# Kernel tuning notes

Measured on AMD Instinct MI355X. Metric: run time of the kernel, lower is better.

The kernel has to match this reference:

```python
import jax, jax.numpy as jnp
import numpy as np

B, T, F, U = 32, 2048, 1024, 512


def setup_inputs() -> dict:
    key = jax.random.key(0)
    k1, k2, k3, k4, k5 = jax.random.split(key, 5)
    return {
        "x": jax.random.normal(k1, (B, T, F), dtype=jnp.float32),
        "W": jax.random.normal(k2, (F, U), dtype=jnp.float32) / np.sqrt(F),
        "b": jnp.zeros((U,), dtype=jnp.float32),
        "transitions": jax.random.normal(k3, (U, U), dtype=jnp.float32),
        "left_boundary": jax.random.normal(k4, (U,), dtype=jnp.float32) * 0.1,
        "right_boundary": jax.random.normal(k5, (U,), dtype=jnp.float32) * 0.1,
    }


def _add_boundary_energy(potentials, start, end):
    # mask=None path: add start to first timestep, end to last timestep
    first = potentials[:, :1, :] + start[None, None, :]
    last = potentials[:, -1:, :] + end[None, None, :]
    return jnp.concatenate([first, potentials[:, 1:-1, :], last], axis=1)


def _crf_decode(potentials, transitions):
    # Viterbi decode (tfa.text.crf_decode), full sequence lengths.
    # potentials: [B, T, U], transitions: [U, U]
    state0 = potentials[:, 0]                       # [B, U]
    rest = jnp.swapaxes(potentials[:, 1:], 0, 1)    # [T-1, B, U]

    def fwd(state, pot_t):
        # scores[b, i, j] = state[b, i] + transitions[i, j]
        scores = state[:, :, None] + transitions[None, :, :]  # [B, U, U]
        bp = jnp.argmax(scores, axis=1).astype(jnp.int32)     # [B, U]
        new_state = jnp.max(scores, axis=1) + pot_t
        return new_state, bp

    final_state, bps = jax.lax.scan(fwd, state0, rest)  # bps: [T-1, B, U]
    last_tag = jnp.argmax(final_state, axis=-1).astype(jnp.int32)  # [B]

    def back(tag, bp):
        prev = jnp.take_along_axis(bp, tag[:, None], axis=1)[:, 0]
        return prev, prev

    _, tags = jax.lax.scan(back, last_tag, bps, reverse=True)  # [T-1, B]
    seq = jnp.concatenate([tags, last_tag[None, :]], axis=0)   # [T, B]
    return jnp.swapaxes(seq, 0, 1)                             # [B, T]


def reference(x, W, b, transitions, left_boundary, right_boundary):
    potentials = jnp.einsum("btf,fu->btu", x, W) + b           # Dense(units)
    potentials = _add_boundary_energy(potentials, left_boundary, right_boundary)
    sequence_lengths = jnp.full((x.shape[0],), x.shape[1], dtype=jnp.int64)
    viterbi_sequence = _crf_decode(potentials, transitions)
    return viterbi_sequence, potentials, sequence_lengths, transitions
```

## Files before the change

### kernel.cpp

```cpp
#include <hip/hip_runtime.h>
#include <cstddef>

#define U_DIM 512
#define T_DIM 2048
#define B_DIM 32
#define F_DIM 1024
#define M_DIM (B_DIM * T_DIM)
#define NBLK 8
#define UB (U_DIM / NBLK)

#define BM 128
#define BN 64
#define BK 16

__global__ __launch_bounds__(256) void gemm_kernel(
    const float* __restrict__ x, const float* __restrict__ W,
    const float* __restrict__ bias, const float* __restrict__ lb,
    const float* __restrict__ rb, float* __restrict__ out)
{
  __shared__ float As[BK][BM + 4];
  __shared__ float Bs[BK][BN];
  const int m0 = blockIdx.x * BM;
  const int n0 = blockIdx.y * BN;
  const int tid = threadIdx.x;
  const int tx = tid & 15;
  const int ty = tid >> 4;

  float acc[8][4];
#pragma unroll
  for (int i = 0; i < 8; ++i)
#pragma unroll
    for (int j = 0; j < 4; ++j) acc[i][j] = 0.f;

  for (int k0 = 0; k0 < F_DIM; k0 += BK) {
#pragma unroll
    for (int i = 0; i < 2; ++i) {
      int id = i * 256 + tid;
      int row = id >> 2;
      int c4 = (id & 3) << 2;
      float4 a = *(const float4*)(x + (size_t)(m0 + row) * F_DIM + k0 + c4);
      As[c4 + 0][row] = a.x;
      As[c4 + 1][row] = a.y;
      As[c4 + 2][row] = a.z;
      As[c4 + 3][row] = a.w;
    }
    {
      int krow = tid >> 4;
      int c4 = (tid & 15) << 2;
      *(float4*)(&Bs[krow][c4]) =
          *(const float4*)(W + (size_t)(k0 + krow) * U_DIM + n0 + c4);
    }
    __syncthreads();
#pragma unroll
    for (int k = 0; k < BK; ++k) {
      float a[8], bb[4];
#pragma unroll
      for (int i = 0; i < 8; ++i) a[i] = As[k][ty * 8 + i];
#pragma unroll
      for (int j = 0; j < 4; ++j) bb[j] = Bs[k][tx * 4 + j];
#pragma unroll
      for (int i = 0; i < 8; ++i)
#pragma unroll
        for (int j = 0; j < 4; ++j) acc[i][j] += a[i] * bb[j];
    }
    __syncthreads();
  }

#pragma unroll
  for (int i = 0; i < 8; ++i) {
    int m = m0 + ty * 8 + i;
    int t = m & (T_DIM - 1);
    float4 o;
#pragma unroll
    for (int j = 0; j < 4; ++j) {
      int n = n0 + tx * 4 + j;
      float v = acc[i][j] + bias[n];
      if (t == 0) v += lb[n];
      if (t == T_DIM - 1) v += rb[n];
      ((float*)&o)[j] = v;
    }
    *(float4*)(out + (size_t)m * U_DIM + n0 + tx * 4) = o;
  }
}

__global__ void aux_kernel(const float* __restrict__ tr, float* __restrict__ out_tr,
                           float* __restrict__ trT, float* __restrict__ seqlen)
{
  int idx = blockIdx.x * blockDim.x + threadIdx.x;
  if (idx < U_DIM * U_DIM) {
    float v = tr[idx];
    out_tr[idx] = v;
    int r = idx >> 9;
    int c = idx & 511;
    trT[(size_t)c * U_DIM + r] = v;
  }
  if (idx < B_DIM) seqlen[idx] = (float)T_DIM;
}

__global__ void init_kernel(unsigned int* __restrict__ flags)
{
  int i = blockIdx.x * blockDim.x + threadIdx.x;
  if (i < B_DIM * NBLK) flags[i] = 0u;
}

__global__ __launch_bounds__(512) void scan_kernel(
    const float* __restrict__ pot, const float* __restrict__ trT,
    float* __restrict__ stateBuf,
    unsigned int* __restrict__ flags,
    unsigned short* __restrict__ bp,
    float* __restrict__ outv)
{
  const int blk = blockIdx.x;
  const int b = blk & (B_DIM - 1);
  const int j = blk >> 5;
  const int tid = threadIdx.x;
  const int u_local = tid >> 3;
  const int vseg = tid & 7;
  const int u = j * UB + u_local;

  __shared__ float sh_state[U_DIM];
  __shared__ float sh_v[U_DIM];
  __shared__ int sh_i[U_DIM];

  float4 trreg[16];
  const float* trRow = trT + (size_t)u * U_DIM;
#pragma unroll
  for (int m = 0; m < 16; ++m)
    trreg[m] = *(const float4*)(trRow + vseg * 4 + m * 32);

  const float* potb = pot + (size_t)b * T_DIM * U_DIM;
  unsigned int* myflags = flags + b * NBLK;

  for (int t = 1; t < T_DIM; ++t) {
    float p_u = potb[(size_t)t * U_DIM + u];

    if (t > 1) {
      if (tid < NBLK) {
        while (__hip_atomic_load(&myflags[tid], __ATOMIC_RELAXED,
                                 __HIP_MEMORY_SCOPE_AGENT) < (unsigned)(t - 1)) {}
      }
      __syncthreads();
      sh_state[tid] = __hip_atomic_load(
          &stateBuf[(size_t)((t - 1) & 1) * B_DIM * U_DIM +
                    (size_t)b * U_DIM + tid],
          __ATOMIC_RELAXED, __HIP_MEMORY_SCOPE_AGENT);
    } else {
      sh_state[tid] = potb[tid];
    }
    __syncthreads();

    float best = -3.402823466e38f;
    int bi = 0;
#pragma unroll
    for (int m = 0; m < 16; ++m) {
      float4 st = *(const float4*)(&sh_state[vseg * 4 + m * 32]);
      float4 trv = trreg[m];
      int vbase = vseg * 4 + m * 32;
      float s0 = st.x + trv.x;
      float s1 = st.y + trv.y;
      float s2 = st.z + trv.z;
      float s3 = st.w + trv.w;
      if (s0 > best) { best = s0; bi = vbase; }
      if (s1 > best) { best = s1; bi = vbase + 1; }
      if (s2 > best) { best = s2; bi = vbase + 2; }
      if (s3 > best) { best = s3; bi = vbase + 3; }
    }
#pragma unroll
    for (int d = 1; d < 8; d <<= 1) {
      float ob = __shfl_xor(best, d, 64);
      int oi = __shfl_xor(bi, d, 64);
      if (ob > best || (ob == best && oi < bi)) { best = ob; bi = oi; }
    }
    if (vseg == 0) {
      float ns = best + p_u;
      __hip_atomic_store(
          &stateBuf[(size_t)(t & 1) * B_DIM * U_DIM + (size_t)b * U_DIM + u],
          ns, __ATOMIC_RELAXED, __HIP_MEMORY_SCOPE_AGENT);
      __builtin_nontemporal_store(
          (unsigned short)bi,
          &bp[(size_t)(t - 1) * (B_DIM * U_DIM) + (size_t)b * U_DIM + u]);
    }
    __syncthreads();
    if (tid == 0) {
      __hip_atomic_store(&myflags[j], (unsigned int)t, __ATOMIC_RELAXED,
                         __HIP_MEMORY_SCOPE_AGENT);
    }
  }

  __syncthreads();
  if (tid == 0) {
    __builtin_amdgcn_fence(__ATOMIC_RELEASE, "agent");
    __hip_atomic_store(&myflags[j], (unsigned int)T_DIM, __ATOMIC_RELAXED,
                       __HIP_MEMORY_SCOPE_AGENT);
  }

  if (j == 0) {
    if (tid < NBLK) {
      while (__hip_atomic_load(&myflags[tid], __ATOMIC_RELAXED,
                               __HIP_MEMORY_SCOPE_AGENT) < (unsigned)T_DIM) {}
    }
    __syncthreads();
    if (tid == 0) __builtin_amdgcn_fence(__ATOMIC_ACQUIRE, "agent");
    __syncthreads();

    sh_v[tid] = __hip_atomic_load(
        &stateBuf[(size_t)1 * B_DIM * U_DIM + (size_t)b * U_DIM + tid],
        __ATOMIC_RELAXED, __HIP_MEMORY_SCOPE_AGENT);
    sh_i[tid] = tid;
    __syncthreads();
    for (int s = 256; s > 0; s >>= 1) {
      if (tid < s) {
        float a = sh_v[tid], c = sh_v[tid + s];
        int ia = sh_i[tid], ic = sh_i[tid + s];
        if (c > a || (c == a && ic < ia)) { sh_v[tid] = c; sh_i[tid] = ic; }
      }
      __syncthreads();
    }
    if (tid == 0) {
      int tag = sh_i[0];
      outv[(size_t)b * T_DIM + (T_DIM - 1)] = (float)tag;
      for (int t = T_DIM - 1; t >= 1; --t) {
        tag = bp[(size_t)(t - 1) * (B_DIM * U_DIM) + (size_t)b * U_DIM + tag];
        outv[(size_t)b * T_DIM + (t - 1)] = (float)tag;
      }
    }
  }
}

extern "C" void kernel_launch(void* const* d_in, const int* in_sizes, int n_in,
                              void* d_out, int out_size, void* d_ws, size_t ws_size,
                              hipStream_t stream)
{
  const float* x    = (const float*)d_in[0];
  const float* W    = (const float*)d_in[1];
  const float* bias = (const float*)d_in[2];
  const float* tr   = (const float*)d_in[3];
  const float* lb   = (const float*)d_in[4];
  const float* rb   = (const float*)d_in[5];

  float* out = (float*)d_out;
  float* out_v   = out;
  float* out_pot = out + (size_t)B_DIM * T_DIM;
  float* out_seq = out_pot + (size_t)B_DIM * T_DIM * U_DIM;
  float* out_tr  = out_seq + B_DIM;

  float* trT = (float*)d_ws;
  float* stateBuf = trT + (size_t)U_DIM * U_DIM;
  unsigned int* flags = (unsigned int*)(stateBuf + 2 * B_DIM * U_DIM);
  unsigned short* bp = (unsigned short*)(flags + B_DIM * NBLK);

  hipLaunchKernelGGL(init_kernel, dim3(1), dim3(256), 0, stream, flags);
  hipLaunchKernelGGL(aux_kernel, dim3(1024), dim3(256), 0, stream,
                     tr, out_tr, trT, out_seq);
  hipLaunchKernelGGL(gemm_kernel, dim3(M_DIM / BM, U_DIM / BN), dim3(256), 0,
                     stream, x, W, bias, lb, rb, out_pot);
  hipLaunchKernelGGL(scan_kernel, dim3(NBLK * B_DIM), dim3(512), 0, stream,
                     out_pot, trT, stateBuf, flags, bp, out_v);
}
```

Measured before the change: 6.666 ms.

## Replace per-step flag barrier with timestep-tagged packed state words

Each state value is packed with its timestep into a 64-bit word, so consumers poll the state entries directly instead of waiting on per-block flags. This drops the extra __syncthreads and flag store per step and the separate flag-then-data round trip across blocks. It adds a double-buffered shared state array and an init pass to zero the packed buffer. In exchange, every thread now spins on global memory, which may add contention.

```diff
diff --git a/kernel.cpp b/kernel.cpp
--- a/kernel.cpp
+++ b/kernel.cpp
@@ -97,15 +97,17 @@
   if (idx < B_DIM) seqlen[idx] = (float)T_DIM;
 }
 
-__global__ void init_kernel(unsigned int* __restrict__ flags)
+__global__ void init_kernel(unsigned long long* __restrict__ statePk,
+                            unsigned int* __restrict__ flags)
 {
   int i = blockIdx.x * blockDim.x + threadIdx.x;
+  if (i < 2 * B_DIM * U_DIM) statePk[i] = 0ull;
   if (i < B_DIM * NBLK) flags[i] = 0u;
 }
 
 __global__ __launch_bounds__(512) void scan_kernel(
     const float* __restrict__ pot, const float* __restrict__ trT,
-    float* __restrict__ stateBuf,
+    unsigned long long* __restrict__ statePk,
     unsigned int* __restrict__ flags,
     unsigned short* __restrict__ bp,
     float* __restrict__ outv)
@@ -118,7 +120,7 @@
   const int vseg = tid & 7;
   const int u = j * UB + u_local;
 
-  __shared__ float sh_state[U_DIM];
+  __shared__ float sh_state[2][U_DIM];
   __shared__ float sh_v[U_DIM];
   __shared__ int sh_i[U_DIM];
 
@@ -129,23 +131,25 @@
     trreg[m] = *(const float4*)(trRow + vseg * 4 + m * 32);
 
   const float* potb = pot + (size_t)b * T_DIM * U_DIM;
+  unsigned long long* stb = statePk + (size_t)b * U_DIM;
   unsigned int* myflags = flags + b * NBLK;
 
   for (int t = 1; t < T_DIM; ++t) {
+    const int cur = t & 1;
     float p_u = potb[(size_t)t * U_DIM + u];
 
     if (t > 1) {
-      if (tid < NBLK) {
-        while (__hip_atomic_load(&myflags[tid], __ATOMIC_RELAXED,
-                                 __HIP_MEMORY_SCOPE_AGENT) < (unsigned)(t - 1)) {}
-      }
-      __syncthreads();
-      sh_state[tid] = __hip_atomic_load(
-          &stateBuf[(size_t)((t - 1) & 1) * B_DIM * U_DIM +
-                    (size_t)b * U_DIM + tid],
-          __ATOMIC_RELAXED, __HIP_MEMORY_SCOPE_AGENT);
+      const unsigned int want = (unsigned int)(t - 1);
+      unsigned long long w;
+      do {
+        w = __hip_atomic_load(
+            &statePk[(size_t)((t - 1) & 1) * B_DIM * U_DIM +
+                     (size_t)b * U_DIM + tid],
+            __ATOMIC_RELAXED, __HIP_MEMORY_SCOPE_AGENT);
+      } while ((unsigned int)(w >> 32) != want);
+      sh_state[cur][tid] = __uint_as_float((unsigned int)w);
     } else {
-      sh_state[tid] = potb[tid];
+      sh_state[cur][tid] = potb[tid];
     }
     __syncthreads();
 
@@ -153,7 +157,7 @@
     int bi = 0;
 #pragma unroll
     for (int m = 0; m < 16; ++m) {
-      float4 st = *(const float4*)(&sh_state[vseg * 4 + m * 32]);
+      float4 st = *(const float4*)(&sh_state[cur][vseg * 4 + m * 32]);
       float4 trv = trreg[m];
       int vbase = vseg * 4 + m * 32;
       float s0 = st.x + trv.x;
@@ -173,17 +177,15 @@
     }
     if (vseg == 0) {
       float ns = best + p_u;
+      unsigned long long pw =
+          ((unsigned long long)(unsigned int)t << 32) |
+          (unsigned long long)__float_as_uint(ns);
       __hip_atomic_store(
-          &stateBuf[(size_t)(t & 1) * B_DIM * U_DIM + (size_t)b * U_DIM + u],
-          ns, __ATOMIC_RELAXED, __HIP_MEMORY_SCOPE_AGENT);
+          &statePk[(size_t)cur * B_DIM * U_DIM + (size_t)b * U_DIM + u], pw,
+          __ATOMIC_RELAXED, __HIP_MEMORY_SCOPE_AGENT);
       __builtin_nontemporal_store(
           (unsigned short)bi,
           &bp[(size_t)(t - 1) * (B_DIM * U_DIM) + (size_t)b * U_DIM + u]);
-    }
-    __syncthreads();
-    if (tid == 0) {
-      __hip_atomic_store(&myflags[j], (unsigned int)t, __ATOMIC_RELAXED,
-                         __HIP_MEMORY_SCOPE_AGENT);
     }
   }
 
@@ -203,10 +205,14 @@
     if (tid == 0) __builtin_amdgcn_fence(__ATOMIC_ACQUIRE, "agent");
     __syncthreads();
 
-    sh_v[tid] = __hip_atomic_load(
-        &stateBuf[(size_t)1 * B_DIM * U_DIM + (size_t)b * U_DIM + tid],
-        __ATOMIC_RELAXED, __HIP_MEMORY_SCOPE_AGENT);
-    sh_i[tid] = tid;
+    {
+      unsigned long long w = __hip_atomic_load(
+          &statePk[(size_t)((T_DIM - 1) & 1) * B_DIM * U_DIM +
+                   (size_t)b * U_DIM + tid],
+          __ATOMIC_RELAXED, __HIP_MEMORY_SCOPE_AGENT);
+      sh_v[tid] = __uint_as_float((unsigned int)w);
+      sh_i[tid] = tid;
+    }
     __syncthreads();
     for (int s = 256; s > 0; s >>= 1) {
       if (tid < s) {
@@ -245,15 +251,17 @@
   float* out_tr  = out_seq + B_DIM;
 
   float* trT = (float*)d_ws;
-  float* stateBuf = trT + (size_t)U_DIM * U_DIM;
-  unsigned int* flags = (unsigned int*)(stateBuf + 2 * B_DIM * U_DIM);
+  unsigned long long* statePk =
+      (unsigned long long*)(trT + (size_t)U_DIM * U_DIM);
+  unsigned int* flags = (unsigned int*)(statePk + 2 * B_DIM * U_DIM);
   unsigned short* bp = (unsigned short*)(flags + B_DIM * NBLK);
 
-  hipLaunchKernelGGL(init_kernel, dim3(1), dim3(256), 0, stream, flags);
+  hipLaunchKernelGGL(init_kernel, dim3(128), dim3(256), 0, stream,
+                     statePk, flags);
   hipLaunchKernelGGL(aux_kernel, dim3(1024), dim3(256), 0, stream,
                      tr, out_tr, trT, out_seq);
   hipLaunchKernelGGL(gemm_kernel, dim3(M_DIM / BM, U_DIM / BN), dim3(256), 0,
                      stream, x, W, bias, lb, rb, out_pot);
   hipLaunchKernelGGL(scan_kernel, dim3(NBLK * B_DIM), dim3(512), 0, stream,
-                     out_pot, trT, stateBuf, flags, bp, out_v);
-}
+                     out_pot, trT, statePk, flags, bp, out_v);
+}
```

New measurement: 7.158 ms. 7.4% more time.
